# Optimization experiments

Hardware: AMD Instinct MI355X
Metric: run time of the kernel (lower is better)

The kernel has to match this reference:

```python
import jax, jax.numpy as jnp
import numpy as np

DIM = 1024
LN_EPS = 1e-5


def setup_inputs() -> dict:
    key = jax.random.key(0)
    ks = jax.random.split(key, 6)
    B, S, D = 8, 2048, DIM
    x = jax.random.normal(ks[0], (B, S, D), dtype=jnp.float32)
    mask = jnp.ones((B, S, 1), dtype=jnp.float32)
    # LayerNorm params
    ln_g = jnp.ones((D,), dtype=jnp.float32)
    ln_b = jnp.zeros((D,), dtype=jnp.float32)
    # FeedForward: Linear(D, D) -> GELU -> Linear(D, D); hidden_dim == dim per source
    lim = 1.0 / np.sqrt(D)
    w1 = jax.random.uniform(ks[1], (D, D), jnp.float32, -lim, lim)
    b1 = jax.random.uniform(ks[2], (D,), jnp.float32, -lim, lim)
    w2 = jax.random.uniform(ks[3], (D, D), jnp.float32, -lim, lim)
    b2 = jax.random.uniform(ks[4], (D,), jnp.float32, -lim, lim)
    return {"x": x, "mask": mask, "ln_g": ln_g, "ln_b": ln_b,
            "w1": w1, "b1": b1, "w2": w2, "b2": b2}


def _layernorm(t, g, b):
    mu = jnp.mean(t, axis=-1, keepdims=True)
    var = jnp.mean(jnp.square(t - mu), axis=-1, keepdims=True)
    return (t - mu) * jax.lax.rsqrt(var + LN_EPS) * g + b


def reference(x, mask, ln_g, ln_b, w1, b1, w2, b2):
    # torch.fft(t, signal_ndim=1): FFT over hidden axis (complex input, imag=0)
    ft = jnp.fft.fft(x.astype(jnp.float32), axis=-1)
    # torch.fft(., signal_ndim=2): 2D FFT over (seq, hidden)
    ft = jnp.fft.fft2(ft, axes=(-2, -1))
    ft = ft.real  # [..., 0] slice of the fake-complex tensor
    t = _layernorm(x + ft, ln_g, ln_b)
    # FeedForward: Linear -> GELU(exact) -> Linear (dropout is identity at eval)
    h = jax.nn.gelu(t @ w1 + b1, approximate=False)
    out = h @ w2 + b2
    return out * mask
```

## Files before the change

### kernel.cpp

```cpp
#include <hip/hip_runtime.h>
#include <math.h>

#define DIMD 1024
#define SEQ  2048
#define BATCH 8
#define ROWS (BATCH * SEQ)

#define MF 1280
#define KF 1152

typedef __attribute__((ext_vector_type(8))) short bf16x8;
typedef __attribute__((ext_vector_type(4))) float f32x4;
typedef __attribute__((ext_vector_type(8))) unsigned short ushort8;

__device__ __forceinline__ unsigned short f2bf(float f) {
    unsigned u = __float_as_uint(f);
    unsigned r = (u + 0x7FFFu + ((u >> 16) & 1u)) >> 16;
    return (unsigned short)r;
}
__device__ __forceinline__ void gl_lds16(const void* g, void* l) {
    __builtin_amdgcn_global_load_lds(
        (const __attribute__((address_space(1))) unsigned int*)g,
        (__attribute__((address_space(3))) unsigned int*)l, 16, 0, 0);
}


__global__ __launch_bounds__(256) void build_acos(unsigned short* __restrict__ Acos) {
    int s = blockIdx.x;
    for (int t = threadIdx.x; t < KF; t += 256) {
        float c = 0.0f;
        if (t <= 1024) {
            int prod = (s * t) & (SEQ - 1);
            c = 1024.0f * cospif((float)prod * (1.0f / 1024.0f));
        }
        Acos[(size_t)s * KF + t] = f2bf(c);
    }
}

__global__ __launch_bounds__(256) void build_xe(const float* __restrict__ x,
                                                unsigned short* __restrict__ Xe) {
    int lane = threadIdx.x & 63;
    int oct  = threadIdx.x >> 6;
    int n = blockIdx.x * 64 + lane;
    int b = n >> 10, d = n & 1023;
    int rd = (DIMD - d) & (DIMD - 1);
    int t0 = blockIdx.y * 32 + oct * 8;
    const float* xb = x + (size_t)b * SEQ * DIMD + rd;
    ushort8 tmp;
    #pragma unroll
    for (int j = 0; j < 8; ++j) {
        int t = t0 + j;
        float v;
        if (t == 0)          v = xb[0];
        else if (t < 1024)   v = xb[(size_t)t * DIMD] + xb[(size_t)(2048 - t) * DIMD];
        else if (t == 1024)  v = xb[(size_t)1024 * DIMD];
        else                 v = 0.0f;
        tmp[j] = f2bf(v);
    }
    *(ushort8*)&Xe[(size_t)n * KF + t0] = tmp;
}

__global__ __launch_bounds__(256) void pack_wt(const float* __restrict__ W,
                                               unsigned short* __restrict__ Wt) {
    int lane = threadIdx.x & 63;
    int oct = threadIdx.x >> 6;
    int n = blockIdx.x * 64 + lane;
    int k0 = blockIdx.y * 32 + oct * 8;
    ushort8 tmp;
    #pragma unroll
    for (int j = 0; j < 8; ++j) tmp[j] = f2bf(W[(size_t)(k0 + j) * DIMD + n]);
    *(ushort8*)&Wt[(size_t)n * DIMD + k0] = tmp;
}

template <int MODE>
__global__ __launch_bounds__(512, 2) void gemm8p(const unsigned short* __restrict__ A,
                                                 const unsigned short* __restrict__ B,
                                                 int K, int lda, int ldb, int ldc,
                                                 const float* __restrict__ bias,
                                                 const float* __restrict__ mask,
                                                 void* __restrict__ outp) {
    __shared__ unsigned short As[2][256 * 64];
    __shared__ unsigned short Bs[2][256 * 64];

    const int tid  = threadIdx.x;
    const int lane = tid & 63;
    const int w    = tid >> 6;
    const int wm   = w >> 2;
    const int wn   = w & 3;
    const int fr   = lane & 15;
    const int quad = lane >> 4;
    const int sw   = fr & 7;

    const int st_row = lane >> 3;
    const int st_col = ((lane & 7) ^ st_row) * 8;

    int bx = blockIdx.x, by = blockIdx.y;
    if (MODE != 0) {
        int lin = bx + 4 * by;
        int c = lin & 7, r = lin >> 3;
        by = c * 8 + (r >> 2);
        bx = r & 3;
    }
    const int m0 = by * 256;
    const int n0 = bx * 256;

    auto stageA = [&](int buf, int qm, int kt) {
        int kb = kt * 64 + st_col;
        int c0 = qm * 8 + w;
        int c1 = 16 + qm * 8 + w;
        gl_lds16(&A[(size_t)(m0 + c0 * 8 + st_row) * lda + kb], &As[buf][c0 * 512]);
        gl_lds16(&A[(size_t)(m0 + c1 * 8 + st_row) * lda + kb], &As[buf][c1 * 512]);
    };
    auto stageB = [&](int buf, int qn, int kt) {
        int kb = kt * 64 + st_col;
        int c0 = (w >> 1) * 8 + qn * 4 + (w & 1) * 2;
        int c1 = c0 + 1;
        gl_lds16(&B[(size_t)(n0 + c0 * 8 + st_row) * ldb + kb], &Bs[buf][c0 * 512]);
        gl_lds16(&B[(size_t)(n0 + c1 * 8 + st_row) * ldb + kb], &Bs[buf][c1 * 512]);
    };

    f32x4 acc[8][4] = {};

#define PHASE(BUF, QM, QN, STAGE, DOVM)                                              \
    {                                                                                \
        bf16x8 af[4][2], bv[2][2];                                                   \
        _Pragma("unroll") for (int i = 0; i < 4; ++i) {                              \
            const unsigned short* ab = &As[BUF][(wm * 128 + QM * 64 + i * 16 + fr) * 64]; \
            _Pragma("unroll") for (int ks = 0; ks < 2; ++ks)                         \
                af[i][ks] = *(const bf16x8*)&ab[((ks * 4 + quad) ^ sw) * 8];         \
        }                                                                            \
        _Pragma("unroll") for (int j = 0; j < 2; ++j) {                              \
            const unsigned short* bb = &Bs[BUF][(wn * 64 + QN * 32 + j * 16 + fr) * 64]; \
            _Pragma("unroll") for (int ks = 0; ks < 2; ++ks)                         \
                bv[j][ks] = *(const bf16x8*)&bb[((ks * 4 + quad) ^ sw) * 8];         \
        }                                                                            \
        STAGE;                                                                       \
        asm volatile("s_waitcnt lgkmcnt(8)");                                        \
        __builtin_amdgcn_s_barrier();                                                \
        asm volatile("s_waitcnt lgkmcnt(0)");                                        \
        __builtin_amdgcn_s_setprio(1);                                               \
        _Pragma("unroll") for (int i = 0; i < 4; ++i)                                \
            _Pragma("unroll") for (int j = 0; j < 2; ++j)                            \
                _Pragma("unroll") for (int ks = 0; ks < 2; ++ks)                     \
                    acc[QM * 4 + i][QN * 2 + j] = __builtin_amdgcn_mfma_f32_16x16x32_bf16( \
                        af[i][ks], bv[j][ks], acc[QM * 4 + i][QN * 2 + j], 0, 0, 0); \
        __builtin_amdgcn_s_setprio(0);                                               \
        if (DOVM) asm volatile("s_waitcnt vmcnt(4)" ::: "memory");                   \
        __builtin_amdgcn_s_barrier();                                                \
    }

    const int NT  = K >> 6;
    const int NIT = NT >> 1;

    stageA(0, 0, 0); stageB(0, 0, 0); stageA(0, 1, 0); stageB(0, 1, 0);
    stageA(1, 0, 1); stageB(1, 0, 1);
    asm volatile("s_waitcnt vmcnt(4)" ::: "memory");
    __builtin_amdgcn_s_barrier();

    for (int i = 0; i < NIT; ++i) {
        int t1 = 2 * i + 1;
        int t2 = 2 * i + 2; if (t2 >= NT) t2 = NT - 2;
        int t3 = 2 * i + 3; if (t3 >= NT) t3 = NT - 2;
        PHASE(0, 0, 0, stageA(1, 1, t1), 0)
        PHASE(0, 0, 1, stageB(1, 1, t1), 0)
        PHASE(0, 1, 0, stageA(0, 0, t2), 0)
        PHASE(0, 1, 1, stageB(0, 0, t2), 1)
        PHASE(1, 0, 0, stageA(0, 1, t2), 0)
        PHASE(1, 0, 1, stageB(0, 1, t2), 0)
        PHASE(1, 1, 0, stageA(1, 0, t3), 0)
        PHASE(1, 1, 1, stageB(1, 0, t3), 1)
    }
#undef PHASE

    #pragma unroll
    for (int mi = 0; mi < 8; ++mi) {
        int rowb = m0 + wm * 128 + mi * 16 + quad * 4;
        #pragma unroll
        for (int nj = 0; nj < 4; ++nj) {
            int col = n0 + wn * 64 + nj * 16 + fr;
            float bcol = (MODE != 0) ? bias[col] : 0.0f;
            #pragma unroll
            for (int r = 0; r < 4; ++r) {
                float v = acc[mi][nj][r];
                int row = rowb + r;
                if (MODE == 0) {
                    ((float*)outp)[(size_t)row * ldc + col] = v;
                } else if (MODE == 1) {
                    v += bcol;
                    v = 0.5f * v * (1.0f + erff(v * 0.70710678118654752f));
                    ((unsigned short*)outp)[(size_t)row * ldc + col] = f2bf(v);
                } else {
                    v += bcol;
                    v *= mask[row];
                    ((float*)outp)[(size_t)row * ldc + col] = v;
                }
            }
        }
    }
}

__global__ __launch_bounds__(256) void ln_pair(const float* __restrict__ x,
                                               const float* __restrict__ F,
                                               const float* __restrict__ g,
                                               const float* __restrict__ beta,
                                               unsigned short* __restrict__ t) {
    const int sp = blockIdx.x;
    const int b  = blockIdx.y;

    float4 fv = ((const float4*)(F + (size_t)sp * 8192 + (size_t)b * 1024))[threadIdx.x];
    float4 g4 = ((const float4*)g)[threadIdx.x];
    float4 b4 = ((const float4*)beta)[threadIdx.x];

    __shared__ float red[4];
    const int wave = threadIdx.x >> 6;
    const int lane = threadIdx.x & 63;

    const int nrows = (sp >= 1 && sp <= 1023) ? 2 : 1;
    for (int p = 0; p < nrows; ++p) {
        int s = p ? (2048 - sp) : sp;
        int row = b * SEQ + s;
        float4 xv = ((const float4*)(x + (size_t)row * DIMD))[threadIdx.x];
        float v0 = xv.x + fv.x, v1 = xv.y + fv.y, v2 = xv.z + fv.z, v3 = xv.w + fv.w;

        float sm = v0 + v1 + v2 + v3;
        #pragma unroll
        for (int off = 32; off > 0; off >>= 1) sm += __shfl_down(sm, off, 64);
        if (lane == 0) red[wave] = sm;
        __syncthreads();
        const float mean = (red[0] + red[1] + red[2] + red[3]) * (1.0f / DIMD);

        float dx0 = v0 - mean, dx1 = v1 - mean, dx2 = v2 - mean, dx3 = v3 - mean;
        float q = dx0 * dx0 + dx1 * dx1 + dx2 * dx2 + dx3 * dx3;
        __syncthreads();
        #pragma unroll
        for (int off = 32; off > 0; off >>= 1) q += __shfl_down(q, off, 64);
        if (lane == 0) red[wave] = q;
        __syncthreads();
        const float var = (red[0] + red[1] + red[2] + red[3]) * (1.0f / DIMD);
        const float rstd = rsqrtf(var + 1e-5f);

        ushort4 o;
        o.x = f2bf(dx0 * rstd * g4.x + b4.x);
        o.y = f2bf(dx1 * rstd * g4.y + b4.y);
        o.z = f2bf(dx2 * rstd * g4.z + b4.z);
        o.w = f2bf(dx3 * rstd * g4.w + b4.w);
        ((ushort4*)(t + (size_t)row * DIMD))[threadIdx.x] = o;
        __syncthreads();
    }
}

#define BM 64
#define BN 64
#define BK 16

__global__ __launch_bounds__(256) void fft_cos_kernel(const float* __restrict__ x,
                                                      float* __restrict__ y) {
    __shared__ float tab[SEQ];
    __shared__ float As[BM][BK + 1];
    __shared__ float Bs[BK][BN + 1];
    const int tid = threadIdx.x;
    const int b = blockIdx.z;
    const int s0 = blockIdx.y * BM;
    const int n0 = blockIdx.x * BN;
    for (int i = tid; i < SEQ; i += 256) tab[i] = cospif((float)i * (1.0f / 1024.0f));
    const int tx = tid & 15;
    const int ty = tid >> 4;
    float acc[4][4] = {};
    const float* Xb = x + (size_t)b * SEQ * DIMD;
    for (int k0 = 0; k0 < SEQ; k0 += BK) {
        __syncthreads();
        for (int f = tid; f < BM * BK; f += 256) {
            int i = f / BK, k = f % BK;
            int prod = (s0 + i) * (k0 + k);
            As[i][k] = tab[prod & (SEQ - 1)];
        }
        for (int f = tid; f < BK * BN; f += 256) {
            int k = f / BN, j = f % BN;
            int d = n0 + j;
            int rd = (DIMD - d) & (DIMD - 1);
            Bs[k][j] = Xb[(size_t)(k0 + k) * DIMD + rd];
        }
        __syncthreads();
        #pragma unroll
        for (int k = 0; k < BK; ++k) {
            float a[4], bv[4];
            #pragma unroll
            for (int i = 0; i < 4; ++i) a[i] = As[ty * 4 + i][k];
            #pragma unroll
            for (int j = 0; j < 4; ++j) bv[j] = Bs[k][tx * 4 + j];
            #pragma unroll
            for (int i = 0; i < 4; ++i)
                #pragma unroll
                for (int j = 0; j < 4; ++j) acc[i][j] += a[i] * bv[j];
        }
    }
    #pragma unroll
    for (int i = 0; i < 4; ++i) {
        int s = s0 + ty * 4 + i;
        #pragma unroll
        for (int j = 0; j < 4; ++j) {
            int d = n0 + tx * 4 + j;
            y[((size_t)b * SEQ + s) * DIMD + d] = Xb[(size_t)s * DIMD + d] + 1024.0f * acc[i][j];
        }
    }
}

__global__ __launch_bounds__(256) void ln_kernel(float* __restrict__ y,
                                                 const float* __restrict__ g,
                                                 const float* __restrict__ beta) {
    const int row = blockIdx.x;
    float4* p = (float4*)(y + (size_t)row * DIMD);
    float4 v = p[threadIdx.x];
    __shared__ float red[4];
    const int wave = threadIdx.x >> 6;
    const int lane = threadIdx.x & 63;
    float s = v.x + v.y + v.z + v.w;
    #pragma unroll
    for (int off = 32; off > 0; off >>= 1) s += __shfl_down(s, off, 64);
    if (lane == 0) red[wave] = s;
    __syncthreads();
    const float mean = (red[0] + red[1] + red[2] + red[3]) * (1.0f / DIMD);
    float dx0 = v.x - mean, dx1 = v.y - mean, dx2 = v.z - mean, dx3 = v.w - mean;
    float q = dx0 * dx0 + dx1 * dx1 + dx2 * dx2 + dx3 * dx3;
    __syncthreads();
    #pragma unroll
    for (int off = 32; off > 0; off >>= 1) q += __shfl_down(q, off, 64);
    if (lane == 0) red[wave] = q;
    __syncthreads();
    const float var = (red[0] + red[1] + red[2] + red[3]) * (1.0f / DIMD);
    const float rstd = rsqrtf(var + 1e-5f);
    float4 g4 = ((const float4*)g)[threadIdx.x];
    float4 b4 = ((const float4*)beta)[threadIdx.x];
    float4 o;
    o.x = dx0 * rstd * g4.x + b4.x;
    o.y = dx1 * rstd * g4.y + b4.y;
    o.z = dx2 * rstd * g4.z + b4.z;
    o.w = dx3 * rstd * g4.w + b4.w;
    p[threadIdx.x] = o;
}

template <int MODE>
__global__ __launch_bounds__(256) void ff_gemm(const float* __restrict__ A,
                                               const float* __restrict__ W,
                                               const float* __restrict__ bias,
                                               const float* __restrict__ mask,
                                               float* __restrict__ out) {
    __shared__ float As[BM][BK + 1];
    __shared__ float Bs[BK][BN + 1];
    const int tid = threadIdx.x;
    const int tx = tid & 15;
    const int ty = tid >> 4;
    const int m0 = blockIdx.y * BM;
    const int n0 = blockIdx.x * BN;
    float acc[4][4] = {};
    for (int k0 = 0; k0 < DIMD; k0 += BK) {
        __syncthreads();
        for (int f = tid; f < BM * BK; f += 256) {
            int i = f / BK, k = f % BK;
            As[i][k] = A[(size_t)(m0 + i) * DIMD + k0 + k];
        }
        for (int f = tid; f < BK * BN; f += 256) {
            int k = f / BN, j = f % BN;
            Bs[k][j] = W[(size_t)(k0 + k) * DIMD + n0 + j];
        }
        __syncthreads();
        #pragma unroll
        for (int k = 0; k < BK; ++k) {
            float a[4], bv[4];
            #pragma unroll
            for (int i = 0; i < 4; ++i) a[i] = As[ty * 4 + i][k];
            #pragma unroll
            for (int j = 0; j < 4; ++j) bv[j] = Bs[k][tx * 4 + j];
            #pragma unroll
            for (int i = 0; i < 4; ++i)
                #pragma unroll
                for (int j = 0; j < 4; ++j) acc[i][j] += a[i] * bv[j];
        }
    }
    #pragma unroll
    for (int i = 0; i < 4; ++i) {
        int m = m0 + ty * 4 + i;
        float mk = (MODE == 1) ? mask[m] : 1.0f;
        #pragma unroll
        for (int j = 0; j < 4; ++j) {
            int n = n0 + tx * 4 + j;
            float v = acc[i][j] + bias[n];
            if (MODE == 0) v = 0.5f * v * (1.0f + erff(v * 0.70710678118654752f));
            else v *= mk;
            out[(size_t)m * DIMD + n] = v;
        }
    }
}

extern "C" void kernel_launch(void* const* d_in, const int* in_sizes, int n_in,
                              void* d_out, int out_size, void* d_ws, size_t ws_size,
                              hipStream_t stream) {
    const float* x    = (const float*)d_in[0];
    const float* mask = (const float*)d_in[1];
    const float* ln_g = (const float*)d_in[2];
    const float* ln_b = (const float*)d_in[3];
    const float* w1   = (const float*)d_in[4];
    const float* b1   = (const float*)d_in[5];
    const float* w2   = (const float*)d_in[6];
    const float* b2   = (const float*)d_in[7];
    float* out = (float*)d_out;

    const size_t MB = 1024 * 1024;
    dim3 blk(256);
    dim3 blk512(512);

    if (ws_size >= 70 * MB) {
        char* w = (char*)d_ws;
        unsigned short* Acos = (unsigned short*)w;
        unsigned short* Xe   = (unsigned short*)(w + 4 * MB);
        unsigned short* t    = (unsigned short*)(w + 32 * MB);
        unsigned short* h    = (unsigned short*)w;
        unsigned short* W1t  = (unsigned short*)(w + 64 * MB);
        unsigned short* W2t  = (unsigned short*)(w + 66 * MB);
        float* F = (float*)d_out;

        build_acos<<<dim3(MF), blk, 0, stream>>>(Acos);
        build_xe<<<dim3(8192 / 64, KF / 32), blk, 0, stream>>>(x, Xe);
        pack_wt<<<dim3(1024 / 64, 1024 / 32), blk, 0, stream>>>(w1, W1t);
        pack_wt<<<dim3(1024 / 64, 1024 / 32), blk, 0, stream>>>(w2, W2t);

        gemm8p<0><<<dim3(8192 / 256, MF / 256), blk512, 0, stream>>>(
            Acos, Xe, KF, KF, KF, 8192, nullptr, nullptr, F);
        ln_pair<<<dim3(1025, BATCH), blk, 0, stream>>>(x, F, ln_g, ln_b, t);
        gemm8p<1><<<dim3(1024 / 256, ROWS / 256), blk512, 0, stream>>>(
            t, W1t, 1024, 1024, 1024, 1024, b1, nullptr, h);
        gemm8p<2><<<dim3(1024 / 256, ROWS / 256), blk512, 0, stream>>>(
            h, W2t, 1024, 1024, 1024, 1024, b2, mask, out);
    } else {
        float* yf = (float*)d_ws;
        const size_t bufBytes = (size_t)ROWS * DIMD * sizeof(float);
        fft_cos_kernel<<<dim3(DIMD / BN, SEQ / BM, BATCH), blk, 0, stream>>>(x, yf);
        ln_kernel<<<dim3(ROWS), blk, 0, stream>>>(yf, ln_g, ln_b);
        ff_gemm<0><<<dim3(DIMD / BN, ROWS / BM), blk, 0, stream>>>(yf, w1, b1, nullptr, out);
        ff_gemm<1><<<dim3(DIMD / BN, ROWS / BM), blk, 0, stream>>>(out, w2, b2, mask, yf);
        hipMemcpyAsync(d_out, yf, bufBytes, hipMemcpyDeviceToDevice, stream);
    }
}
```

Before: 321.8 us.

## Double-buffer LDS fragment reads across GEMM phases to overlap with MFMAs

Restructures the GEMM main loop so each phase issues LDS reads for the next phase's A/B fragments into a second register set while running MFMAs on the current set. This is meant to hide LDS read latency behind matrix math instead of waiting on lgkmcnt before computing. The vmcnt fence moves to the start of the phase that reads a freshly staged buffer. The cost is higher register pressure from two fragment sets, and the new fence placement is subtle enough that the staging order could race.

```diff
diff --git a/kernel.cpp b/kernel.cpp
--- a/kernel.cpp
+++ b/kernel.cpp
@@ -121,31 +121,33 @@
 
     f32x4 acc[8][4] = {};
 
-#define PHASE(BUF, QM, QN, STAGE, DOVM)                                              \
+    bf16x8 afA[4][2], bvA[2][2], afB[4][2], bvB[2][2];
+
+#define READS(NAF, NBV, BUFR, QMR, QNR, KS)                                          \
+    _Pragma("unroll") for (int i = 0; i < 4; ++i)                                    \
+        NAF[i][KS] = *(const bf16x8*)&As[BUFR][(wm * 128 + QMR * 64 + i * 16 + fr) * 64 \
+                                              + (((KS * 4 + quad) ^ sw) * 8)];       \
+    _Pragma("unroll") for (int j = 0; j < 2; ++j)                                    \
+        NBV[j][KS] = *(const bf16x8*)&Bs[BUFR][(wn * 64 + QNR * 32 + j * 16 + fr) * 64 \
+                                              + (((KS * 4 + quad) ^ sw) * 8)];
+
+#define MFMAS(CAF, CBV, QMC, QNC, KS)                                                \
+    _Pragma("unroll") for (int i = 0; i < 4; ++i)                                    \
+        _Pragma("unroll") for (int j = 0; j < 2; ++j)                                \
+            acc[QMC * 4 + i][QNC * 2 + j] = __builtin_amdgcn_mfma_f32_16x16x32_bf16( \
+                CAF[i][KS], CBV[j][KS], acc[QMC * 4 + i][QNC * 2 + j], 0, 0, 0);
+
+#define PHASE(CAF, CBV, NAF, NBV, QMC, QNC, BUFR, QMR, QNR, STAGE, FENCE)            \
     {                                                                                \
-        bf16x8 af[4][2], bv[2][2];                                                   \
-        _Pragma("unroll") for (int i = 0; i < 4; ++i) {                              \
-            const unsigned short* ab = &As[BUF][(wm * 128 + QM * 64 + i * 16 + fr) * 64]; \
-            _Pragma("unroll") for (int ks = 0; ks < 2; ++ks)                         \
-                af[i][ks] = *(const bf16x8*)&ab[((ks * 4 + quad) ^ sw) * 8];         \
-        }                                                                            \
-        _Pragma("unroll") for (int j = 0; j < 2; ++j) {                              \
-            const unsigned short* bb = &Bs[BUF][(wn * 64 + QN * 32 + j * 16 + fr) * 64]; \
-            _Pragma("unroll") for (int ks = 0; ks < 2; ++ks)                         \
-                bv[j][ks] = *(const bf16x8*)&bb[((ks * 4 + quad) ^ sw) * 8];         \
-        }                                                                            \
+        if (FENCE) asm volatile("s_waitcnt vmcnt(2)" ::: "memory");                  \
         STAGE;                                                                       \
-        asm volatile("s_waitcnt lgkmcnt(8)");                                        \
-        __builtin_amdgcn_s_barrier();                                                \
-        asm volatile("s_waitcnt lgkmcnt(0)");                                        \
+        READS(NAF, NBV, BUFR, QMR, QNR, 0)                                           \
         __builtin_amdgcn_s_setprio(1);                                               \
-        _Pragma("unroll") for (int i = 0; i < 4; ++i)                                \
-            _Pragma("unroll") for (int j = 0; j < 2; ++j)                            \
-                _Pragma("unroll") for (int ks = 0; ks < 2; ++ks)                     \
-                    acc[QM * 4 + i][QN * 2 + j] = __builtin_amdgcn_mfma_f32_16x16x32_bf16( \
-                        af[i][ks], bv[j][ks], acc[QM * 4 + i][QN * 2 + j], 0, 0, 0); \
+        MFMAS(CAF, CBV, QMC, QNC, 0)                                                 \
+        READS(NAF, NBV, BUFR, QMR, QNR, 1)                                           \
+        MFMAS(CAF, CBV, QMC, QNC, 1)                                                 \
         __builtin_amdgcn_s_setprio(0);                                               \
-        if (DOVM) asm volatile("s_waitcnt vmcnt(4)" ::: "memory");                   \
+        asm volatile("s_waitcnt lgkmcnt(0)" ::: "memory");                           \
         __builtin_amdgcn_s_barrier();                                                \
     }
 
@@ -156,21 +158,27 @@
     stageA(1, 0, 1); stageB(1, 0, 1);
     asm volatile("s_waitcnt vmcnt(4)" ::: "memory");
     __builtin_amdgcn_s_barrier();
+    READS(afA, bvA, 0, 0, 0, 0)
+    READS(afA, bvA, 0, 0, 0, 1)
+    asm volatile("s_waitcnt lgkmcnt(0)" ::: "memory");
+    __builtin_amdgcn_s_barrier();
 
     for (int i = 0; i < NIT; ++i) {
         int t1 = 2 * i + 1;
         int t2 = 2 * i + 2; if (t2 >= NT) t2 = NT - 2;
         int t3 = 2 * i + 3; if (t3 >= NT) t3 = NT - 2;
-        PHASE(0, 0, 0, stageA(1, 1, t1), 0)
-        PHASE(0, 0, 1, stageB(1, 1, t1), 0)
-        PHASE(0, 1, 0, stageA(0, 0, t2), 0)
-        PHASE(0, 1, 1, stageB(0, 0, t2), 1)
-        PHASE(1, 0, 0, stageA(0, 1, t2), 0)
-        PHASE(1, 0, 1, stageB(0, 1, t2), 0)
-        PHASE(1, 1, 0, stageA(1, 0, t3), 0)
-        PHASE(1, 1, 1, stageB(1, 0, t3), 1)
+        PHASE(afA, bvA, afB, bvB, 0, 0, 0, 0, 1, stageA(1, 1, t1), 0)
+        PHASE(afB, bvB, afA, bvA, 0, 1, 0, 1, 0, stageB(1, 1, t1), 0)
+        PHASE(afA, bvA, afB, bvB, 1, 0, 0, 1, 1, stageA(0, 0, t2), 0)
+        PHASE(afB, bvB, afA, bvA, 1, 1, 1, 0, 0, stageB(0, 0, t2), 1)
+        PHASE(afA, bvA, afB, bvB, 0, 0, 1, 0, 1, stageA(0, 1, t2), 0)
+        PHASE(afB, bvB, afA, bvA, 0, 1, 1, 1, 0, stageB(0, 1, t2), 0)
+        PHASE(afA, bvA, afB, bvB, 1, 0, 1, 1, 1, stageA(1, 0, t3), 0)
+        PHASE(afB, bvB, afA, bvA, 1, 1, 0, 0, 0, stageB(1, 0, t3), 1)
     }
 #undef PHASE
+#undef MFMAS
+#undef READS
 
     #pragma unroll
     for (int mi = 0; mi < 8; ++mi) {
```

Result: slower. 330.3 us (+2.7%).

## Switch GEMMs to 32x32x16 MFMA with simpler double-buffered K loop

Applied to the files above, without the earlier changes.

Replaces the 16x16x32 MFMA tiles with 32x32x16 bf16 MFMA, cutting LDS fragment reads per FLOP, and replaces the eight-phase staggered staging pipeline with a simple per-K-tile double buffer that stages all of A and B once per iteration. It also shrinks the padded FFT K dimension from 1152 to 1088, removing some GEMM work. The simpler schedule waits for all loads each iteration, which may expose more memory latency than the previous fine-grained pipeline. The smaller KF must still cover the required FFT terms, and build_acos and build_xe are sized by KF.

```diff
diff --git a/kernel.cpp b/kernel.cpp
--- a/kernel.cpp
+++ b/kernel.cpp
@@ -7,10 +7,11 @@
 #define ROWS (BATCH * SEQ)
 
 #define MF 1280
-#define KF 1152
+#define KF 1088
 
 typedef __attribute__((ext_vector_type(8))) short bf16x8;
 typedef __attribute__((ext_vector_type(4))) float f32x4;
+typedef __attribute__((ext_vector_type(16))) float f32x16;
 typedef __attribute__((ext_vector_type(8))) unsigned short ushort8;
 
 __device__ __forceinline__ unsigned short f2bf(float f) {
@@ -73,7 +74,7 @@
 }
 
 template <int MODE>
-__global__ __launch_bounds__(512, 2) void gemm8p(const unsigned short* __restrict__ A,
+__global__ __launch_bounds__(512, 2) void gemm32(const unsigned short* __restrict__ A,
                                                  const unsigned short* __restrict__ B,
                                                  int K, int lda, int ldb, int ldc,
                                                  const float* __restrict__ bias,
@@ -87,9 +88,9 @@
     const int w    = tid >> 6;
     const int wm   = w >> 2;
     const int wn   = w & 3;
-    const int fr   = lane & 15;
-    const int quad = lane >> 4;
-    const int sw   = fr & 7;
+    const int r31  = lane & 31;
+    const int hl   = lane >> 5;
+    const int sw   = lane & 7;
 
     const int st_row = lane >> 3;
     const int st_col = ((lane & 7) ^ st_row) * 8;
@@ -104,85 +105,77 @@
     const int m0 = by * 256;
     const int n0 = bx * 256;
 
-    auto stageA = [&](int buf, int qm, int kt) {
+    const int rA = wm * 128 + r31;
+    const int rB = wn * 64 + r31;
+
+    auto stage = [&](int buf, int kt) {
         int kb = kt * 64 + st_col;
-        int c0 = qm * 8 + w;
-        int c1 = 16 + qm * 8 + w;
-        gl_lds16(&A[(size_t)(m0 + c0 * 8 + st_row) * lda + kb], &As[buf][c0 * 512]);
-        gl_lds16(&A[(size_t)(m0 + c1 * 8 + st_row) * lda + kb], &As[buf][c1 * 512]);
+        #pragma unroll
+        for (int c = 0; c < 4; ++c) {
+            int ch = w + c * 8;
+            gl_lds16(&A[(size_t)(m0 + ch * 8 + st_row) * lda + kb], &As[buf][ch * 512]);
+            gl_lds16(&B[(size_t)(n0 + ch * 8 + st_row) * ldb + kb], &Bs[buf][ch * 512]);
+        }
     };
-    auto stageB = [&](int buf, int qn, int kt) {
-        int kb = kt * 64 + st_col;
-        int c0 = (w >> 1) * 8 + qn * 4 + (w & 1) * 2;
-        int c1 = c0 + 1;
-        gl_lds16(&B[(size_t)(n0 + c0 * 8 + st_row) * ldb + kb], &Bs[buf][c0 * 512]);
-        gl_lds16(&B[(size_t)(n0 + c1 * 8 + st_row) * ldb + kb], &Bs[buf][c1 * 512]);
-    };
-
-    f32x4 acc[8][4] = {};
-
-#define PHASE(BUF, QM, QN, STAGE, DOVM)                                              \
+
+    f32x16 acc[4][2] = {};
+    bf16x8 a0[4], b0[2], a1[4], b1[2];
+
+#define READK(SA, SB, PA, PB, KK)                                                    \
     {                                                                                \
-        bf16x8 af[4][2], bv[2][2];                                                   \
-        _Pragma("unroll") for (int i = 0; i < 4; ++i) {                              \
-            const unsigned short* ab = &As[BUF][(wm * 128 + QM * 64 + i * 16 + fr) * 64]; \
-            _Pragma("unroll") for (int ks = 0; ks < 2; ++ks)                         \
-                af[i][ks] = *(const bf16x8*)&ab[((ks * 4 + quad) ^ sw) * 8];         \
-        }                                                                            \
-        _Pragma("unroll") for (int j = 0; j < 2; ++j) {                              \
-            const unsigned short* bb = &Bs[BUF][(wn * 64 + QN * 32 + j * 16 + fr) * 64]; \
-            _Pragma("unroll") for (int ks = 0; ks < 2; ++ks)                         \
-                bv[j][ks] = *(const bf16x8*)&bb[((ks * 4 + quad) ^ sw) * 8];         \
-        }                                                                            \
-        STAGE;                                                                       \
-        asm volatile("s_waitcnt lgkmcnt(8)");                                        \
-        __builtin_amdgcn_s_barrier();                                                \
-        asm volatile("s_waitcnt lgkmcnt(0)");                                        \
-        __builtin_amdgcn_s_setprio(1);                                               \
-        _Pragma("unroll") for (int i = 0; i < 4; ++i)                                \
-            _Pragma("unroll") for (int j = 0; j < 2; ++j)                            \
-                _Pragma("unroll") for (int ks = 0; ks < 2; ++ks)                     \
-                    acc[QM * 4 + i][QN * 2 + j] = __builtin_amdgcn_mfma_f32_16x16x32_bf16( \
-                        af[i][ks], bv[j][ks], acc[QM * 4 + i][QN * 2 + j], 0, 0, 0); \
-        __builtin_amdgcn_s_setprio(0);                                               \
-        if (DOVM) asm volatile("s_waitcnt vmcnt(4)" ::: "memory");                   \
-        __builtin_amdgcn_s_barrier();                                                \
-    }
-
-    const int NT  = K >> 6;
-    const int NIT = NT >> 1;
-
-    stageA(0, 0, 0); stageB(0, 0, 0); stageA(0, 1, 0); stageB(0, 1, 0);
-    stageA(1, 0, 1); stageB(1, 0, 1);
-    asm volatile("s_waitcnt vmcnt(4)" ::: "memory");
+        const int so_ = ((((KK) * 2) + hl) ^ sw) * 8;                                \
+        _Pragma("unroll") for (int bi = 0; bi < 4; ++bi)                             \
+            SA[bi] = *(const bf16x8*)&(PA)[(rA + bi * 32) * 64 + so_];               \
+        _Pragma("unroll") for (int bj = 0; bj < 2; ++bj)                             \
+            SB[bj] = *(const bf16x8*)&(PB)[(rB + bj * 32) * 64 + so_];               \
+    }
+
+#define MFMAK(SA, SB)                                                                \
+    __builtin_amdgcn_s_setprio(1);                                                   \
+    _Pragma("unroll") for (int bi = 0; bi < 4; ++bi)                                 \
+        _Pragma("unroll") for (int bj = 0; bj < 2; ++bj)                             \
+            acc[bi][bj] = __builtin_amdgcn_mfma_f32_32x32x16_bf16(                   \
+                SA[bi], SB[bj], acc[bi][bj], 0, 0, 0);                               \
+    __builtin_amdgcn_s_setprio(0);
+
+    const int NT = K >> 6;
+
+    stage(0, 0);
+    asm volatile("s_waitcnt vmcnt(0)" ::: "memory");
     __builtin_amdgcn_s_barrier();
 
-    for (int i = 0; i < NIT; ++i) {
-        int t1 = 2 * i + 1;
-        int t2 = 2 * i + 2; if (t2 >= NT) t2 = NT - 2;
-        int t3 = 2 * i + 3; if (t3 >= NT) t3 = NT - 2;
-        PHASE(0, 0, 0, stageA(1, 1, t1), 0)
-        PHASE(0, 0, 1, stageB(1, 1, t1), 0)
-        PHASE(0, 1, 0, stageA(0, 0, t2), 0)
-        PHASE(0, 1, 1, stageB(0, 0, t2), 1)
-        PHASE(1, 0, 0, stageA(0, 1, t2), 0)
-        PHASE(1, 0, 1, stageB(0, 1, t2), 0)
-        PHASE(1, 1, 0, stageA(1, 0, t3), 0)
-        PHASE(1, 1, 1, stageB(1, 0, t3), 1)
-    }
-#undef PHASE
-
-    #pragma unroll
-    for (int mi = 0; mi < 8; ++mi) {
-        int rowb = m0 + wm * 128 + mi * 16 + quad * 4;
-        #pragma unroll
-        for (int nj = 0; nj < 4; ++nj) {
-            int col = n0 + wn * 64 + nj * 16 + fr;
+    int cur = 0;
+    for (int t = 0; t < NT; ++t) {
+        const unsigned short* pa = &As[cur][0];
+        const unsigned short* pb = &Bs[cur][0];
+        int nk = (t + 1 < NT) ? t + 1 : NT - 1;
+        READK(a0, b0, pa, pb, 0)
+        stage(cur ^ 1, nk);
+        READK(a1, b1, pa, pb, 1)
+        MFMAK(a0, b0)
+        READK(a0, b0, pa, pb, 2)
+        MFMAK(a1, b1)
+        READK(a1, b1, pa, pb, 3)
+        MFMAK(a0, b0)
+        MFMAK(a1, b1)
+        asm volatile("s_waitcnt vmcnt(0) lgkmcnt(0)" ::: "memory");
+        __builtin_amdgcn_s_barrier();
+        cur ^= 1;
+    }
+#undef MFMAK
+#undef READK
+
+    #pragma unroll
+    for (int bi = 0; bi < 4; ++bi) {
+        int rowb = m0 + wm * 128 + bi * 32 + 4 * hl;
+        #pragma unroll
+        for (int bj = 0; bj < 2; ++bj) {
+            int col = n0 + wn * 64 + bj * 32 + r31;
             float bcol = (MODE != 0) ? bias[col] : 0.0f;
             #pragma unroll
-            for (int r = 0; r < 4; ++r) {
-                float v = acc[mi][nj][r];
-                int row = rowb + r;
+            for (int r = 0; r < 16; ++r) {
+                float v = acc[bi][bj][r];
+                int row = rowb + (r & 3) + 8 * (r >> 2);
                 if (MODE == 0) {
                     ((float*)outp)[(size_t)row * ldc + col] = v;
                 } else if (MODE == 1) {
@@ -424,12 +417,12 @@
         pack_wt<<<dim3(1024 / 64, 1024 / 32), blk, 0, stream>>>(w1, W1t);
         pack_wt<<<dim3(1024 / 64, 1024 / 32), blk, 0, stream>>>(w2, W2t);
 
-        gemm8p<0><<<dim3(8192 / 256, MF / 256), blk512, 0, stream>>>(
+        gemm32<0><<<dim3(8192 / 256, MF / 256), blk512, 0, stream>>>(
             Acos, Xe, KF, KF, KF, 8192, nullptr, nullptr, F);
         ln_pair<<<dim3(1025, BATCH), blk, 0, stream>>>(x, F, ln_g, ln_b, t);
-        gemm8p<1><<<dim3(1024 / 256, ROWS / 256), blk512, 0, stream>>>(
+        gemm32<1><<<dim3(1024 / 256, ROWS / 256), blk512, 0, stream>>>(
             t, W1t, 1024, 1024, 1024, 1024, b1, nullptr, h);
-        gemm8p<2><<<dim3(1024 / 256, ROWS / 256), blk512, 0, stream>>>(
+        gemm32<2><<<dim3(1024 / 256, ROWS / 256), blk512, 0, stream>>>(
             h, W2t, 1024, 1024, 1024, 1024, b2, mask, out);
     } else {
         float* yf = (float*)d_ws;
```

Result: faster. 307.9 us (-4.3%).
